# Optimization experiments

Measured on AMD Instinct MI355X. Metric: run time of the kernel, lower is better.

## Reference

```python
import jax, jax.numpy as jnp
import numpy as np

B, T, I, H = 64, 512, 512, 1024

def setup_inputs() -> dict:
    key = jax.random.key(0)
    ks = jax.random.split(key, 5)
    stdv = 1.0 / np.sqrt(H)
    return {
        "x": jax.random.normal(ks[0], (B, T, I), dtype=jnp.float32),
        "w_ih": jax.random.uniform(ks[1], (I, H), jnp.float32, -stdv, stdv),
        "w_hh": jax.random.uniform(ks[2], (H, H), jnp.float32, -stdv, stdv),
        "b_ih": jax.random.uniform(ks[3], (H,), jnp.float32, -stdv, stdv),
        "b_hh": jax.random.uniform(ks[4], (H,), jnp.float32, -stdv, stdv),
    }

def reference(x, w_ih, w_hh, b_ih, b_hh):
    # Precompute input projection for all timesteps (parallel GEMM),
    # then scan over time for the sequential hidden recurrence.
    xw = jnp.einsum('bti,ih->bth', x, w_ih) + (b_ih + b_hh)  # [B,T,H]
    h0 = jnp.zeros((x.shape[0], w_hh.shape[0]), dtype=x.dtype)

    def step(h, xt):  # xt: [B,H]
        h_new = jnp.tanh(xt + h @ w_hh)
        return h_new, h_new

    hT, hs = jax.lax.scan(step, h0, jnp.swapaxes(xw, 0, 1))  # hs: [T,B,H]
    hidden_seq = jnp.swapaxes(hs, 0, 1)  # [B,T,H] (batch_first=True)
    h_t = hT[None]  # [num_layers*D=1, B, H]
    return hidden_seq, h_t
```

## Files before the change

### kernel.cpp

```cpp
#include <hip/hip_runtime.h>
#include <cstdint>
#include <cstddef>

#define B_  64
#define T_  512
#define I_  512
#define H_  1024

typedef float  f32x4  __attribute__((ext_vector_type(4)));
typedef __bf16 bf16x8 __attribute__((ext_vector_type(8)));
typedef unsigned short us4v __attribute__((ext_vector_type(4)));
typedef unsigned int  u32x4 __attribute__((ext_vector_type(4)));
typedef unsigned long long ull;

__device__ __forceinline__ unsigned short f2bf(float f) {
  unsigned int u = __float_as_uint(f);
  u = (u + 0x7fffu + ((u >> 16) & 1u)) >> 16;
  return (unsigned short)u;
}

__device__ __forceinline__ float fast_tanh(float x) {
  x = fminf(10.f, fmaxf(-10.f, x));
  float e = __expf(2.f * x);
  return (e - 1.f) * __builtin_amdgcn_rcpf(e + 1.f);
}

__device__ __forceinline__ void st_ag64(ull* p, ull v) {
  __hip_atomic_store(p, v, __ATOMIC_RELAXED, __HIP_MEMORY_SCOPE_AGENT);
}
__device__ __forceinline__ ull ld_ag64(const ull* p) {
  return __hip_atomic_load(p, __ATOMIC_RELAXED, __HIP_MEMORY_SCOPE_AGENT);
}

__global__ __launch_bounds__(256) void k_transpose_cvt(
    const float* __restrict__ in, unsigned short* __restrict__ out, int R, int C) {
  __shared__ float tile[64][65];
  const int tx = threadIdx.x & 63, ty = threadIdx.x >> 6;
  const int c0 = blockIdx.x * 64, r0 = blockIdx.y * 64;
#pragma unroll
  for (int i = 0; i < 16; i++) {
    int r = i * 4 + ty;
    tile[r][tx] = in[(size_t)(r0 + r) * C + c0 + tx];
  }
  __syncthreads();
#pragma unroll
  for (int i = 0; i < 16; i++) {
    int c = i * 4 + ty;
    out[(size_t)(c0 + c) * R + r0 + tx] = f2bf(tile[tx][c]);
  }
}

__global__ __launch_bounds__(256) void k_prep(
    const float* __restrict__ bih, const float* __restrict__ bhh,
    float* __restrict__ bias) {
  int gid = blockIdx.x * 256 + threadIdx.x;
  if (gid < H_) bias[gid] = bih[gid] + bhh[gid];
}

__global__ __launch_bounds__(256) void k_gemm_xw(
    const float* __restrict__ x, const unsigned short* __restrict__ wihT,
    const float* __restrict__ bias, float* __restrict__ out) {
  __shared__ __align__(16) unsigned short As[128 * 40];
  __shared__ __align__(16) unsigned short Bs[128 * 40];

  const int tid = threadIdx.x;
  const int tileM = blockIdx.x >> 3;
  const int tileN = blockIdx.x & 7;
  const int wv = tid >> 6, lane = tid & 63;
  const int row16 = lane & 15, quad = lane >> 4;
  const int m0 = (wv & 1) * 64, n0 = (wv >> 1) * 64;

  f32x4 acc[4][4];
#pragma unroll
  for (int i = 0; i < 4; i++)
#pragma unroll
    for (int j = 0; j < 4; j++) acc[i][j] = (f32x4){0.f, 0.f, 0.f, 0.f};

  const int ar = tid >> 3, ac = (tid & 7) << 2;
  const int br = tid >> 2, bc = (tid & 3) << 3;

#pragma unroll 1
  for (int kt = 0; kt < I_ / 32; kt++) {
    const int k0 = kt * 32;
#pragma unroll
    for (int i = 0; i < 4; i++) {
      int r = ar + i * 32;
      float4 v = *(const float4*)(x + (size_t)(tileM * 128 + r) * I_ + k0 + ac);
      us4v o;
      o.x = f2bf(v.x); o.y = f2bf(v.y); o.z = f2bf(v.z); o.w = f2bf(v.w);
      *(us4v*)(As + r * 40 + ac) = o;
    }
#pragma unroll
    for (int i = 0; i < 2; i++) {
      int r = br + i * 64;
      *(uint4*)(Bs + r * 40 + bc) =
          *(const uint4*)(wihT + (size_t)(tileN * 128 + r) * I_ + k0 + bc);
    }
    __syncthreads();

    bf16x8 af[4], bfr[4];
#pragma unroll
    for (int mt = 0; mt < 4; mt++)
      af[mt] = *(const bf16x8*)(As + (m0 + mt * 16 + row16) * 40 + quad * 8);
#pragma unroll
    for (int nt = 0; nt < 4; nt++)
      bfr[nt] = *(const bf16x8*)(Bs + (n0 + nt * 16 + row16) * 40 + quad * 8);
#pragma unroll
    for (int mt = 0; mt < 4; mt++)
#pragma unroll
      for (int nt = 0; nt < 4; nt++)
        acc[mt][nt] = __builtin_amdgcn_mfma_f32_16x16x32_bf16(
            af[mt], bfr[nt], acc[mt][nt], 0, 0, 0);
    __syncthreads();
  }

#pragma unroll
  for (int mt = 0; mt < 4; mt++)
#pragma unroll
    for (int nt = 0; nt < 4; nt++) {
      int gc = tileN * 128 + n0 + nt * 16 + row16;
      float bv = bias[gc];
#pragma unroll
      for (int r = 0; r < 4; r++) {
        int gr = tileM * 128 + m0 + mt * 16 + quad * 4 + r;
        out[(size_t)gr * H_ + gc] = acc[mt][nt][r] + bv;
      }
    }
}

__global__ __launch_bounds__(256, 1) void k_scan(
    const unsigned short* __restrict__ whhT,
    unsigned short* __restrict__ hbuf,
    float* __restrict__ out) {
  const int bid = blockIdx.x;
  const int g = bid >> 4, j = bid & 15;
  const int tid = threadIdx.x;
  const int wv = tid >> 6, lane = tid & 63;
  const int row = lane & 15, quad = lane >> 4;
  const int bsl = g * 16;
  const int mycol = j * 64 + wv * 16 + row;

  ull* hb = (ull*)hbuf;
  ull* gbase = hb + g * 16384;

  __shared__ __align__(16) unsigned int ldsb[2 * 16 * 516];

  bf16x8 wfrag[32];
  {
    const unsigned short* wp = whhT + (size_t)mycol * H_ + quad * 8;
#pragma unroll
    for (int kk = 0; kk < 32; kk++)
      wfrag[kk] = *(const bf16x8*)(wp + kk * 32);
  }

  float xwv[4];
  size_t oi[4];
#pragma unroll
  for (int r = 0; r < 4; r++) {
    int b = bsl + quad * 4 + r;
    oi[r] = ((size_t)b * T_) * H_ + mycol;
    xwv[r] = out[oi[r]];
  }

  for (int t = 0; t < T_; ++t) {
    f32x4 acc[4];
#pragma unroll
    for (int c = 0; c < 4; c++) acc[c] = (f32x4){0.f, 0.f, 0.f, 0.f};

    if (t > 0) {
      const ull* src = gbase + ((t - 1) & 1) * 8192;
      const unsigned int expect = (unsigned int)t;
      unsigned int pay[32];
      bool ok;
      do {
        ok = true;
#pragma unroll
        for (int i = 0; i < 32; i++) {
          ull q = ld_ag64(src + i * 256 + tid);
          pay[i] = (unsigned int)q;
          ok &= ((unsigned int)(q >> 32) == expect);
        }
      } while (__builtin_expect(!ok, 0));

      unsigned int* lw = ldsb + (t & 1) * (16 * 516);
#pragma unroll
      for (int i = 0; i < 32; i++)
        lw[(i >> 1) * 516 + (i & 1) * 256 + tid] = pay[i];
      __syncthreads();

      const unsigned int* ap = lw + row * 516 + quad * 4;
#pragma unroll
      for (int kb = 0; kb < 32; kb++) {
        u32x4 w = *(const u32x4*)(ap + kb * 16);
        bf16x8 a = __builtin_bit_cast(bf16x8, w);
        acc[kb & 3] = __builtin_amdgcn_mfma_f32_16x16x32_bf16(
            a, wfrag[kb], acc[kb & 3], 0, 0, 0);
      }
    }
    f32x4 accf = (acc[0] + acc[1]) + (acc[2] + acc[3]);

    float hv[4];
    ull* dst = gbase + (t & 1) * 8192;
    const ull tagbits = ((ull)(unsigned int)(t + 1)) << 32;
#pragma unroll
    for (int r = 0; r < 4; r++) {
      float h = fast_tanh(accf[r] + xwv[r]);
      hv[r] = h;
      unsigned int myu = (unsigned int)f2bf(h);
      unsigned int pr  = __shfl_xor(myu, 1);
      unsigned int pair = myu | (pr << 16);
      if ((lane & 1) == 0) {
        int b = quad * 4 + r;
        st_ag64(dst + b * 512 + (mycol >> 1), tagbits | (ull)pair);
      }
    }
    __builtin_amdgcn_sched_barrier(0);

#pragma unroll
    for (int r = 0; r < 4; r++) {
      out[oi[r]] = hv[r];
      if (t == T_ - 1) {
        int b = bsl + quad * 4 + r;
        out[(size_t)B_ * T_ * H_ + (size_t)b * H_ + mycol] = hv[r];
      }
    }
    if (t + 1 < T_) {
#pragma unroll
      for (int r = 0; r < 4; r++) {
        oi[r] += H_;
        xwv[r] = out[oi[r]];
      }
    }
  }
}

extern "C" void kernel_launch(void* const* d_in, const int* in_sizes, int n_in,
                              void* d_out, int out_size, void* d_ws, size_t ws_size,
                              hipStream_t stream) {
  const float* x    = (const float*)d_in[0];
  const float* w_ih = (const float*)d_in[1];
  const float* w_hh = (const float*)d_in[2];
  const float* b_ih = (const float*)d_in[3];
  const float* b_hh = (const float*)d_in[4];
  float* out = (float*)d_out;

  char* ws = (char*)d_ws;
  unsigned short* whhT = (unsigned short*)(ws);
  unsigned short* wihT = (unsigned short*)(ws + (2u << 20));
  float*          bias = (float*)(ws + (3u << 20));
  unsigned short* hbuf = (unsigned short*)(ws + (3u << 20) + 4096);

  hipLaunchKernelGGL(k_transpose_cvt, dim3(H_ / 64, H_ / 64), dim3(256), 0, stream,
                     w_hh, whhT, H_, H_);
  hipLaunchKernelGGL(k_transpose_cvt, dim3(H_ / 64, I_ / 64), dim3(256), 0, stream,
                     w_ih, wihT, I_, H_);
  hipLaunchKernelGGL(k_prep, dim3(4), dim3(256), 0, stream, b_ih, b_hh, bias);
  hipLaunchKernelGGL(k_gemm_xw, dim3((B_ * T_ / 128) * (H_ / 128)), dim3(256), 0,
                     stream, x, wihT, bias, out);
  hipLaunchKernelGGL(k_scan, dim3(64), dim3(256), 0, stream, whhT, hbuf, out);
}
```

Before: 2.112 ms.

## Prefetch next-step hidden state right after publishing, and swizzle GEMM tile order

The scan kernel now issues the 32 tagged loads for the next timestep's hidden state right after storing its own outputs, before the output writes and the xw reload. The spin-wait then checks the already-loaded tags first and reloads only if some are stale, so the first poll's latency overlaps other work. The input-projection GEMM also remaps block IDs so that groups of eight M-tiles share each N-tile, which should improve cache reuse of the weights. The first poll now comes earlier, so it is more likely to see stale tags and need a second round of loads.

```diff
diff --git a/kernel.cpp b/kernel.cpp
--- a/kernel.cpp
+++ b/kernel.cpp
@@ -64,8 +64,9 @@
   __shared__ __align__(16) unsigned short Bs[128 * 40];
 
   const int tid = threadIdx.x;
-  const int tileM = blockIdx.x >> 3;
-  const int tileN = blockIdx.x & 7;
+  const int bid = blockIdx.x;
+  const int tileM = ((bid >> 6) << 3) | (bid & 7);
+  const int tileN = (bid >> 3) & 7;
   const int wv = tid >> 6, lane = tid & 63;
   const int row16 = lane & 15, quad = lane >> 4;
   const int m0 = (wv & 1) * 64, n0 = (wv >> 1) * 64;
@@ -162,6 +163,8 @@
     xwv[r] = out[oi[r]];
   }
 
+  ull q[32];
+
   for (int t = 0; t < T_; ++t) {
     f32x4 acc[4];
 #pragma unroll
@@ -170,22 +173,21 @@
     if (t > 0) {
       const ull* src = gbase + ((t - 1) & 1) * 8192;
       const unsigned int expect = (unsigned int)t;
-      unsigned int pay[32];
-      bool ok;
-      do {
-        ok = true;
-#pragma unroll
-        for (int i = 0; i < 32; i++) {
-          ull q = ld_ag64(src + i * 256 + tid);
-          pay[i] = (unsigned int)q;
-          ok &= ((unsigned int)(q >> 32) == expect);
-        }
-      } while (__builtin_expect(!ok, 0));
+      for (;;) {
+        unsigned int bad = 0u;
+#pragma unroll
+        for (int i = 0; i < 32; i++)
+          bad |= ((unsigned int)(q[i] >> 32)) ^ expect;
+        if (__builtin_expect(!bad, 1)) break;
+#pragma unroll
+        for (int i = 0; i < 32; i++)
+          q[i] = ld_ag64(src + i * 256 + tid);
+      }
 
       unsigned int* lw = ldsb + (t & 1) * (16 * 516);
 #pragma unroll
       for (int i = 0; i < 32; i++)
-        lw[(i >> 1) * 516 + (i & 1) * 256 + tid] = pay[i];
+        lw[(i >> 1) * 516 + (i & 1) * 256 + tid] = (unsigned int)q[i];
       __syncthreads();
 
       const unsigned int* ap = lw + row * 516 + quad * 4;
@@ -214,6 +216,13 @@
         st_ag64(dst + b * 512 + (mycol >> 1), tagbits | (ull)pair);
       }
     }
+
+    if (t + 1 < T_) {
+      const ull* nsrc = gbase + (t & 1) * 8192;
+#pragma unroll
+      for (int i = 0; i < 32; i++)
+        q[i] = ld_ag64(nsrc + i * 256 + tid);
+    }
     __builtin_amdgcn_sched_barrier(0);
 
 #pragma unroll
```

Result: slower. 2.676 ms (+26.7%).
